# Optimization experiments

Measured on AMD Instinct MI355X. Metric: run time of the kernel, lower is better.

## Reference

```python
import jax, jax.numpy as jnp
import numpy as np

K = 5  # kernel_size per dim
# 2^dim = 4 active degree-1 B-spline products per edge (dim=2)
BITS = jnp.array([[0, 0], [1, 0], [0, 1], [1, 1]], dtype=jnp.int32)  # [S,2]


def spline_basis(edge_attr):
    """Open B-spline basis, degree=1, dim=2, kernel_size=5 per dim.
    Returns basis weights [E,S] and flattened kernel indices [E,S]."""
    v = edge_attr * (K - 1)                 # scale pseudo-coords to knot grid
    i0 = jnp.floor(v)
    f = v - i0                              # fractional part, [E,2]
    # per-dim linear weights: f for bit=1, (1-f) for bit=0
    w = jnp.where(BITS[None] == 1, f[:, None, :], 1.0 - f[:, None, :])  # [E,S,2]
    basis = w[..., 0] * w[..., 1]           # [E,S]
    idx = jnp.minimum(i0.astype(jnp.int32)[:, None, :] + BITS[None], K - 1)  # [E,S,2]
    kidx = idx[..., 0] + K * idx[..., 1]    # flatten 2D kernel index -> [0,25)
    return basis, kidx


def spline_conv(x, src, dst, basis, kidx, W, root, bias, n):
    # transform-then-gather: y[n,k,:] = x[n] @ W[k]
    y = jnp.einsum('ni,kio->nko', x, W)                 # [N,25,out]
    g = y[src[:, None], kidx]                           # gather [E,S,out]
    msg = jnp.einsum('es,eso->eo', basis, g)            # weighted sum over S
    agg = jax.ops.segment_sum(msg, dst, num_segments=n)  # scatter-add to targets
    return agg + x @ root + bias                        # root weight + bias


def setup_inputs() -> dict:
    key = jax.random.key(0)
    ks = jax.random.split(key, 8)
    N, E, IN, H, OUT = 50000, 400000, 32, 64, 64
    x = jax.random.normal(ks[0], (N, IN), jnp.float32)
    edge_index = jax.random.randint(ks[1], (2, E), 0, N, dtype=jnp.int32)
    edge_attr = jax.random.uniform(ks[2], (E, 2), jnp.float32)

    def glorot(k, shape):
        fan = shape[-2] + shape[-1]
        return jax.random.normal(k, shape, jnp.float32) * jnp.sqrt(2.0 / fan)

    W1 = glorot(ks[3], (K * K, IN, H));  root1 = glorot(ks[4], (IN, H));  b1 = jnp.zeros((H,), jnp.float32)
    W2 = glorot(ks[5], (K * K, H, OUT)); root2 = glorot(ks[6], (H, OUT)); b2 = jnp.zeros((OUT,), jnp.float32)
    fc_w = glorot(ks[7], (OUT, 3));      fc_b = jnp.zeros((3,), jnp.float32)
    return dict(x=x, edge_index=edge_index, edge_attr=edge_attr,
                W1=W1, root1=root1, b1=b1, W2=W2, root2=root2, b2=b2,
                fc_w=fc_w, fc_b=fc_b)


def reference(x, edge_index, edge_attr, W1, root1, b1, W2, root2, b2, fc_w, fc_b):
    # eval-mode forward (dropout is identity at inference)
    n = x.shape[0]
    src, dst = edge_index[0], edge_index[1]
    basis, kidx = spline_basis(edge_attr)
    h = jax.nn.relu(spline_conv(x, src, dst, basis, kidx, W1, root1, b1, n))
    h = jax.nn.relu(spline_conv(h, src, dst, basis, kidx, W2, root2, b2, n))
    return h @ fc_w + fc_b
```

## Files before the change

kernel.cpp:

```cpp
#include <hip/hip_runtime.h>
#include <stdint.h>

typedef __attribute__((ext_vector_type(8))) short short8;
typedef __attribute__((ext_vector_type(4))) float f32x4;
typedef __attribute__((ext_vector_type(4))) unsigned short ushort4v;

#define CHUNK 512

__device__ __forceinline__ unsigned short f2bf(float f) {
    unsigned int u = __float_as_uint(f);
    u = (u + 0x7FFFu + ((u >> 16) & 1u)) >> 16;
    return (unsigned short)u;
}
__device__ __forceinline__ float bf2f(unsigned short h) {
    return __uint_as_float(((unsigned int)h) << 16);
}
__device__ __forceinline__ int cell_of(float ax, float ay) {
    int c0 = (int)floorf(ax * 4.f); c0 = min(max(c0, 0), 3);
    int c1 = (int)floorf(ay * 4.f); c1 = min(max(c1, 0), 3);
    return c0 + 4 * c1;
}

__global__ __launch_bounds__(256) void zero_kernel(int* __restrict__ p, int n) {
    int t = blockIdx.x * 256 + threadIdx.x;
    if (t < n) p[t] = 0;
}

template<int KIN>
__device__ __forceinline__ void pack_cell_elem(const float* __restrict__ W,
                                               unsigned short* __restrict__ pkc, int u) {
    constexpr int KCH = KIN / 8;
    if (u >= 16 * 4 * KCH * 512) return;
    int low9 = u & 511;
    int grp  = u >> 9;
    int kc = grp % KCH; grp /= KCH;
    int c  = grp & 3;
    int cell = grp >> 2;
    int lane = low9 >> 3, j = low9 & 7;
    int k = kc * 32 + (lane >> 4) * 8 + j;
    int t = k / KIN, i = k % KIN;
    int k0 = (cell & 3) + (t & 1);   if (k0 > 4) k0 = 4;
    int k1 = (cell >> 2) + (t >> 1); if (k1 > 4) k1 = 4;
    float val = W[((size_t)(k0 + 5 * k1) * KIN + i) * 64 + (c * 16 + (lane & 15))];
    pkc[u] = f2bf(val);
}

template<int KIN>
__device__ __forceinline__ void pack_root_elem(const float* __restrict__ root,
                                               unsigned short* __restrict__ pkr, int u) {
    constexpr int KCHr = KIN / 32;
    if (u >= 4 * KCHr * 512) return;
    int low9 = u & 511;
    int grp  = u >> 9;
    int lane = low9 >> 3, j = low9 & 7;
    int kc = grp % KCHr, c = grp / KCHr;
    int k = kc * 32 + (lane >> 4) * 8 + j;
    int o = c * 16 + (lane & 15);
    float v = root[(size_t)k * 64 + o];
    unsigned short h = f2bf(v);
    pkr[(size_t)(grp * 2) * 512 + low9]     = h;
    pkr[(size_t)(grp * 2 + 1) * 512 + low9] = f2bf(v - bf2f(h));
}

__global__ __launch_bounds__(256) void prep_kernel(
    const float* __restrict__ attr, const int* __restrict__ dst,
    int* __restrict__ hist, int* __restrict__ dhist, int E,
    const float* __restrict__ W1, const float* __restrict__ W2,
    const float* __restrict__ root1, const float* __restrict__ root2,
    unsigned short* __restrict__ pkc1, unsigned short* __restrict__ pkc2,
    unsigned short* __restrict__ pkr1, unsigned short* __restrict__ pkr2,
    const float* __restrict__ x, unsigned short* __restrict__ xb, int n4,
    int EB)
{
    __shared__ int wcnt[4][16];
    int b = blockIdx.x;
    if (b < EB) {
        int e = b * 256 + threadIdx.x;
        int lane = threadIdx.x & 63, wave = threadIdx.x >> 6;
        int cell = -1;
        if (e < E) {
            float2 a = reinterpret_cast<const float2*>(attr)[e];
            cell = cell_of(a.x, a.y);
            atomicAdd(&dhist[dst[e]], 1);
        }
        #pragma unroll
        for (int c = 0; c < 16; c++) {
            unsigned long long m = __ballot(cell == c);
            if (lane == 0) wcnt[wave][c] = __popcll(m);
        }
        __syncthreads();
        if (threadIdx.x < 16) {
            int c = threadIdx.x;
            int tot = wcnt[0][c] + wcnt[1][c] + wcnt[2][c] + wcnt[3][c];
            if (tot) atomicAdd(&hist[c], tot);
        }
        return;
    }
    b -= EB;
    if (b < 512)  { pack_cell_elem<32>(W1, pkc1, b * 256 + threadIdx.x); return; }
    b -= 512;
    if (b < 1024) { pack_cell_elem<64>(W2, pkc2, b * 256 + threadIdx.x); return; }
    b -= 1024;
    if (b < 8)    { pack_root_elem<32>(root1, pkr1, b * 256 + threadIdx.x); return; }
    b -= 8;
    if (b < 16)   { pack_root_elem<64>(root2, pkr2, b * 256 + threadIdx.x); return; }
    b -= 16;
    {
        int t = b * 256 + threadIdx.x;
        if (t < n4) {
            float4 v = reinterpret_cast<const float4*>(x)[t];
            ushort4v o = { f2bf(v.x), f2bf(v.y), f2bf(v.z), f2bf(v.w) };
            reinterpret_cast<ushort4v*>(xb)[t] = o;
        }
    }
}

__global__ __launch_bounds__(1024) void scanA_kernel(const int* __restrict__ dhist,
                                                     int* __restrict__ nof,
                                                     int* __restrict__ bsum, int Np1) {
    __shared__ int wsum[16];
    int tid = threadIdx.x, lane = tid & 63, w = tid >> 6;
    int i = blockIdx.x * 1024 + tid;
    int v = (i < Np1) ? dhist[i] : 0;
    int s = v;
    #pragma unroll
    for (int off = 1; off < 64; off <<= 1) {
        int t = __shfl_up(s, off);
        if (lane >= off) s += t;
    }
    if (lane == 63) wsum[w] = s;
    __syncthreads();
    if (tid == 0) {
        int a = 0;
        #pragma unroll
        for (int k = 0; k < 16; k++) { int t = wsum[k]; wsum[k] = a; a += t; }
        bsum[blockIdx.x] = a;
    }
    __syncthreads();
    if (i < Np1) nof[i] = wsum[w] + s - v;
}

__global__ void scan_small_kernel(const int* __restrict__ hist, int* __restrict__ off_e,
                                  int* __restrict__ off_b, int* __restrict__ cursor,
                                  const int* __restrict__ bsum, int* __restrict__ bbase, int NB) {
    if (threadIdx.x == 0 && blockIdx.x == 0) {
        int se = 0, sb = 0;
        for (int c = 0; c < 16; c++) {
            off_e[c] = se; off_b[c] = sb; cursor[c] = se;
            se += hist[c]; sb += (hist[c] + CHUNK - 1) / CHUNK;
        }
        off_e[16] = se; off_b[16] = sb;
        int a = 0;
        for (int bks = 0; bks < NB; bks++) { int t = bsum[bks]; bbase[bks] = a; a += t; }
    }
}

__global__ __launch_bounds__(256) void scatter_kernel(const float* __restrict__ attr,
                                                      const int* __restrict__ src,
                                                      const int* __restrict__ dst,
                                                      const int* __restrict__ nof,
                                                      const int* __restrict__ bbase,
                                                      int4* __restrict__ emeta,
                                                      int* __restrict__ cursor,
                                                      int* __restrict__ dhist, int E) {
    __shared__ int wcnt[4][16];
    __shared__ int wbase[4][16];
    int e = blockIdx.x * 256 + threadIdx.x;
    int lane = threadIdx.x & 63, wave = threadIdx.x >> 6;
    int cell = -1;
    float2 a = {0.f, 0.f};
    int mp = 0, sv = 0;
    if (e < E) {
        a = reinterpret_cast<const float2*>(attr)[e];
        cell = cell_of(a.x, a.y);
        int d = dst[e];
        int rank = atomicSub(&dhist[d], 1) - 1;
        mp = nof[d] + bbase[d >> 10] + rank;
        sv = src[e];
    }
    int myrank = 0;
    #pragma unroll
    for (int c = 0; c < 16; c++) {
        unsigned long long m = __ballot(cell == c);
        if (cell == c) myrank = __popcll(m & ((1ull << lane) - 1ull));
        if (lane == 0) wcnt[wave][c] = __popcll(m);
    }
    __syncthreads();
    if (threadIdx.x < 16) {
        int c = threadIdx.x;
        int t0 = wcnt[0][c], t1 = wcnt[1][c], t2 = wcnt[2][c], t3 = wcnt[3][c];
        int tot = t0 + t1 + t2 + t3;
        int g = tot ? atomicAdd(&cursor[c], tot) : 0;
        wbase[0][c] = g;
        wbase[1][c] = g + t0;
        wbase[2][c] = g + t0 + t1;
        wbase[3][c] = g + t0 + t1 + t2;
    }
    __syncthreads();
    if (e < E) {
        int slot = wbase[wave][cell] + myrank;
        emeta[slot] = make_int4(sv, mp, __float_as_int(a.x), __float_as_int(a.y));
    }
}

template<int KIN>
__global__ __launch_bounds__(256) void layer_kernel(
    const unsigned short* __restrict__ Xb,
    const unsigned short* __restrict__ pkr, float* __restrict__ rt,
    const float* __restrict__ bias, int N, int RG,
    const unsigned short* __restrict__ pkc, unsigned short* __restrict__ msg,
    const int4* __restrict__ emeta,
    const int* __restrict__ off_e, const int* __restrict__ off_b)
{
    constexpr int KCHr = KIN / 32;
    constexpr int KCH  = 4 * KCHr;
    __shared__ unsigned short Blds[4 * KCH * 512];

    const int lane = threadIdx.x & 63;
    const int wave = threadIdx.x >> 6;
    const int lrow = lane & 15, lch = lane >> 4;

    if (blockIdx.x < RG) {
        const int mbase = blockIdx.x * 64 + wave * 16;
        short8 afrag[KCHr];
        {
            int row = mbase + lrow;
            if (row > N - 1) row = N - 1;
            const unsigned short* ap = Xb + (size_t)row * KIN + lch * 8;
            #pragma unroll
            for (int kc = 0; kc < KCHr; kc++)
                afrag[kc] = *reinterpret_cast<const short8*>(ap + kc * 32);
        }
        f32x4 acc[4];
        #pragma unroll
        for (int c = 0; c < 4; c++) acc[c] = (f32x4){0.f, 0.f, 0.f, 0.f};
        #pragma unroll
        for (int c = 0; c < 4; c++) {
            #pragma unroll
            for (int kc = 0; kc < KCHr; kc++) {
                short8 bh = *reinterpret_cast<const short8*>(pkr + ((size_t)(c * KCHr + kc) * 2    ) * 512 + lane * 8);
                short8 bl = *reinterpret_cast<const short8*>(pkr + ((size_t)(c * KCHr + kc) * 2 + 1) * 512 + lane * 8);
                acc[c] = __builtin_amdgcn_mfma_f32_16x16x32_bf16(afrag[kc], bh, acc[c], 0, 0, 0);
                acc[c] = __builtin_amdgcn_mfma_f32_16x16x32_bf16(afrag[kc], bl, acc[c], 0, 0, 0);
            }
        }
        #pragma unroll
        for (int c = 0; c < 4; c++) {
            int o = c * 16 + lrow;
            float bv = bias[o];
            #pragma unroll
            for (int r = 0; r < 4; r++) {
                int m = mbase + lch * 4 + r;
                if (m < N) rt[(size_t)m * 64 + o] = acc[c][r] + bv;
            }
        }
        return;
    }

    const int b = blockIdx.x - RG;
    if (b >= off_b[16]) return;
    int cell = 0;
    #pragma unroll
    for (int c = 1; c < 16; c++) cell += (b >= off_b[c]);
    const int chunk = b - off_b[cell];

    {
        const short8* sp = reinterpret_cast<const short8*>(pkc + (size_t)cell * (4 * KCH * 512));
        short8* dp = reinterpret_cast<short8*>(Blds);
        #pragma unroll
        for (int p = 0; p < (4 * KCH * 512 / 8) / 256; p++)
            dp[p * 256 + threadIdx.x] = sp[p * 256 + threadIdx.x];
    }
    __syncthreads();

    const int ebeg = off_e[cell];
    const int eend = off_e[cell + 1];
    const int base = ebeg + chunk * CHUNK;
    const float c0f = (float)(cell & 3), c1f = (float)(cell >> 2);

    for (int tt = 0; tt < 8; tt++) {
        const int tbase = base + (tt * 4 + wave) * 16;
        if (tbase >= eend) continue;
        const int eslot = tbase + lrow;
        const bool valid = eslot < eend;

        const int4 em = emeta[valid ? eslot : ebeg];
        const int s  = em.x;
        const int mp = valid ? em.y : -1;
        const float ax = __int_as_float(em.z);
        const float ay = __int_as_float(em.w);

        const float f0 = ax * 4.f - c0f;
        const float f1 = ay * 4.f - c1f;
        float w[4] = { (1.f - f0) * (1.f - f1), f0 * (1.f - f1),
                       (1.f - f0) * f1,         f0 * f1 };

        short8 xfrag[KCHr];
        {
            const unsigned short* xp = Xb + (size_t)s * KIN + lch * 8;
            #pragma unroll
            for (int kcr = 0; kcr < KCHr; kcr++)
                xfrag[kcr] = *reinterpret_cast<const short8*>(xp + kcr * 32);
        }

        float wr[4][4];
        int pv[4];
        #pragma unroll
        for (int r = 0; r < 4; r++) {
            int er = lch * 4 + r;
            #pragma unroll
            for (int t = 0; t < 4; t++) wr[t][r] = __shfl(w[t], er);
            pv[r] = __shfl(mp, er);
        }

        #pragma unroll
        for (int ch = 0; ch < 2; ch++) {
            f32x4 accT[4][2];
            #pragma unroll
            for (int t = 0; t < 4; t++)
                #pragma unroll
                for (int c2 = 0; c2 < 2; c2++)
                    accT[t][c2] = (f32x4){0.f, 0.f, 0.f, 0.f};

            #pragma unroll
            for (int t = 0; t < 4; t++) {
                #pragma unroll
                for (int kcr = 0; kcr < KCHr; kcr++) {
                    #pragma unroll
                    for (int c2 = 0; c2 < 2; c2++) {
                        int c = ch * 2 + c2;
                        short8 bf = *reinterpret_cast<const short8*>(
                            &Blds[(size_t)((c * KCH) + (t * KCHr + kcr)) * 512 + lane * 8]);
                        accT[t][c2] = __builtin_amdgcn_mfma_f32_16x16x32_bf16(xfrag[kcr], bf, accT[t][c2], 0, 0, 0);
                    }
                }
            }

            #pragma unroll
            for (int c2 = 0; c2 < 2; c2++) {
                const int o = (ch * 2 + c2) * 16 + lrow;
                #pragma unroll
                for (int r = 0; r < 4; r++) {
                    if (pv[r] >= 0) {
                        float m = wr[0][r] * accT[0][c2][r] + wr[1][r] * accT[1][c2][r]
                                + wr[2][r] * accT[2][c2][r] + wr[3][r] * accT[3][c2][r];
                        msg[(size_t)pv[r] * 64 + o] = f2bf(m);
                    }
                }
            }
        }
    }
}

template<int MODE>
__global__ __launch_bounds__(256) void segsum_kernel(
    const unsigned short* __restrict__ msg, const float* __restrict__ rt,
    const int* __restrict__ nof, const int* __restrict__ bbase,
    unsigned short* __restrict__ hout,
    const float* __restrict__ fcw, const float* __restrict__ fcb,
    float* __restrict__ out, int N)
{
    int n = blockIdx.x * 4 + (threadIdx.x >> 6);
    if (n >= N) return;
    int lane = threadIdx.x & 63;
    float acc = rt[(size_t)n * 64 + lane];
    int jb = nof[n]     + bbase[n >> 10];
    int je = nof[n + 1] + bbase[(n + 1) >> 10];
    int j = jb;
    for (; j + 3 < je; j += 4) {
        float a0 = bf2f(msg[(size_t)(j + 0) * 64 + lane]);
        float a1 = bf2f(msg[(size_t)(j + 1) * 64 + lane]);
        float a2 = bf2f(msg[(size_t)(j + 2) * 64 + lane]);
        float a3 = bf2f(msg[(size_t)(j + 3) * 64 + lane]);
        acc += a0; acc += a1; acc += a2; acc += a3;
    }
    for (; j < je; j++) acc += bf2f(msg[(size_t)j * 64 + lane]);
    acc = fmaxf(acc, 0.f);
    if (MODE == 0) {
        hout[(size_t)n * 64 + lane] = f2bf(acc);
    } else {
        float p0 = acc * fcw[lane * 3 + 0];
        float p1 = acc * fcw[lane * 3 + 1];
        float p2 = acc * fcw[lane * 3 + 2];
        #pragma unroll
        for (int off = 32; off; off >>= 1) {
            p0 += __shfl_xor(p0, off);
            p1 += __shfl_xor(p1, off);
            p2 += __shfl_xor(p2, off);
        }
        if (lane == 0) {
            out[(size_t)n * 3 + 0] = p0 + fcb[0];
            out[(size_t)n * 3 + 1] = p1 + fcb[1];
            out[(size_t)n * 3 + 2] = p2 + fcb[2];
        }
    }
}

extern "C" void kernel_launch(void* const* d_in, const int* in_sizes, int n_in,
                              void* d_out, int out_size, void* d_ws, size_t ws_size,
                              hipStream_t stream)
{
    const float* x     = (const float*)d_in[0];
    const int*   ei    = (const int*)  d_in[1];
    const float* attr  = (const float*)d_in[2];
    const float* W1    = (const float*)d_in[3];
    const float* root1 = (const float*)d_in[4];
    const float* b1    = (const float*)d_in[5];
    const float* W2    = (const float*)d_in[6];
    const float* root2 = (const float*)d_in[7];
    const float* b2    = (const float*)d_in[8];
    const float* fcw   = (const float*)d_in[9];
    const float* fcb   = (const float*)d_in[10];

    const int N = in_sizes[0] / 32;
    const int E = in_sizes[1] / 2;
    const int* srcp = ei;
    const int* dstp = ei + E;

    char* wsp = (char*)d_ws;
    auto alloc = [&](size_t bytes) -> char* {
        char* p = wsp;
        wsp += (bytes + 255) & ~(size_t)255;
        return p;
    };
    const int NB = (N + 1 + 1023) / 1024;

    float*          rt       = (float*)alloc((size_t)N * 64 * 4);
    unsigned short* xb       = (unsigned short*)alloc((size_t)N * 32 * 2);
    unsigned short* h1b      = (unsigned short*)alloc((size_t)N * 64 * 2);
    unsigned short* pkr1     = (unsigned short*)alloc((size_t)4 * 1 * 2 * 512 * 2);
    unsigned short* pkr2     = (unsigned short*)alloc((size_t)4 * 2 * 2 * 512 * 2);
    unsigned short* pkc1     = (unsigned short*)alloc((size_t)16 * 4 * 4 * 512 * 2);
    unsigned short* pkc2     = (unsigned short*)alloc((size_t)16 * 4 * 8 * 512 * 2);
    int4*           emeta    = (int4*)alloc((size_t)E * 16);
    int*            nof      = (int*)alloc((size_t)(N + 1) * 4);
    int*            bsum     = (int*)alloc((size_t)NB * 4);
    int*            bbase    = (int*)alloc((size_t)NB * 4);
    int*            off_e    = (int*)alloc(17 * 4);
    int*            off_b    = (int*)alloc(17 * 4);
    int*            cursor   = (int*)alloc(16 * 4);
    int*            zbase    = (int*)alloc((size_t)(16 + N + 1) * 4);
    int*            hist     = zbase;
    int*            dhist    = zbase + 16;
    unsigned short* msg      = (unsigned short*)alloc((size_t)E * 64 * 2);

    const int ZN = 16 + N + 1;
    zero_kernel<<<(ZN + 255) / 256, 256, 0, stream>>>(zbase, ZN);

    const int EB = (E + 255) / 256;
    const int CB = (N * 8 + 255) / 256;
    const int prep_grid = EB + 512 + 1024 + 8 + 16 + CB;

    prep_kernel<<<prep_grid, 256, 0, stream>>>(attr, dstp, hist, dhist, E,
                                               W1, W2, root1, root2,
                                               pkc1, pkc2, pkr1, pkr2,
                                               x, xb, N * 8, EB);
    scanA_kernel<<<NB, 1024, 0, stream>>>(dhist, nof, bsum, N + 1);
    scan_small_kernel<<<1, 64, 0, stream>>>(hist, off_e, off_b, cursor, bsum, bbase, NB);
    scatter_kernel<<<EB, 256, 0, stream>>>(attr, srcp, dstp, nof, bbase, emeta, cursor, dhist, E);

    const int RG = (N + 63) / 64;
    const int lgrid = RG + (E + CHUNK - 1) / CHUNK + 16;
    const int sgrid = (N + 3) / 4;

    layer_kernel<32><<<lgrid, 256, 0, stream>>>(xb, pkr1, rt, b1, N, RG,
                                                pkc1, msg, emeta, off_e, off_b);
    segsum_kernel<0><<<sgrid, 256, 0, stream>>>(msg, rt, nof, bbase, h1b, fcw, fcb, (float*)d_out, N);

    layer_kernel<64><<<lgrid, 256, 0, stream>>>(h1b, pkr2, rt, b2, N, RG,
                                                pkc2, msg, emeta, off_e, off_b);
    segsum_kernel<1><<<sgrid, 256, 0, stream>>>(msg, rt, nof, bbase, nullptr, fcw, fcb, (float*)d_out, N);
}
```

Before: 181.4 us.

## Process two edge tiles per wave iteration, double chunk size, fuse scan kernels

The layer kernel now handles two 16-edge tiles per wave iteration, so each B fragment loaded from LDS feeds two MFMAs. The chunk size grows to 1024 edges per block to amortise the per-block weight staging into LDS. The two scan kernels are merged into one, using a last-block-done atomic counter, which removes a kernel launch. The trade-off is higher register pressure from the doubled accumulators and fragments, and fewer, larger blocks that may leave some cells underfilled.

```diff
diff --git a/kernel.cpp b/kernel.cpp
--- a/kernel.cpp
+++ b/kernel.cpp
@@ -5,7 +5,7 @@
 typedef __attribute__((ext_vector_type(4))) float f32x4;
 typedef __attribute__((ext_vector_type(4))) unsigned short ushort4v;
 
-#define CHUNK 512
+#define CHUNK 1024
 
 __device__ __forceinline__ unsigned short f2bf(float f) {
     unsigned int u = __float_as_uint(f);
@@ -115,9 +115,12 @@
     }
 }
 
-__global__ __launch_bounds__(1024) void scanA_kernel(const int* __restrict__ dhist,
-                                                     int* __restrict__ nof,
-                                                     int* __restrict__ bsum, int Np1) {
+__global__ __launch_bounds__(1024) void scanAB_kernel(
+    const int* __restrict__ dhist, int* __restrict__ nof, int* __restrict__ bsum,
+    int Np1, int* __restrict__ done,
+    const int* __restrict__ hist, int* __restrict__ off_e, int* __restrict__ off_b,
+    int* __restrict__ cursor, int* __restrict__ bbase, int NB)
+{
     __shared__ int wsum[16];
     int tid = threadIdx.x, lane = tid & 63, w = tid >> 6;
     int i = blockIdx.x * 1024 + tid;
@@ -138,20 +141,27 @@
     }
     __syncthreads();
     if (i < Np1) nof[i] = wsum[w] + s - v;
-}
-
-__global__ void scan_small_kernel(const int* __restrict__ hist, int* __restrict__ off_e,
-                                  int* __restrict__ off_b, int* __restrict__ cursor,
-                                  const int* __restrict__ bsum, int* __restrict__ bbase, int NB) {
-    if (threadIdx.x == 0 && blockIdx.x == 0) {
+
+    __shared__ int amLast;
+    __shared__ int lds_b[256];
+    __shared__ int lds_h[16];
+    __threadfence();
+    if (tid == 0) amLast = (atomicAdd(done, 1) == gridDim.x - 1);
+    __syncthreads();
+    if (!amLast) return;
+    __threadfence();
+    if (tid < NB) lds_b[tid] = bsum[tid];
+    if (tid < 16) lds_h[tid] = hist[tid];
+    __syncthreads();
+    if (tid == 0) {
+        int a = 0;
+        for (int k = 0; k < NB; k++) { int t = lds_b[k]; bbase[k] = a; a += t; }
         int se = 0, sb = 0;
         for (int c = 0; c < 16; c++) {
             off_e[c] = se; off_b[c] = sb; cursor[c] = se;
-            se += hist[c]; sb += (hist[c] + CHUNK - 1) / CHUNK;
+            se += lds_h[c]; sb += (lds_h[c] + CHUNK - 1) / CHUNK;
         }
         off_e[16] = se; off_b[16] = sb;
-        int a = 0;
-        for (int bks = 0; bks < NB; bks++) { int t = bsum[bks]; bbase[bks] = a; a += t; }
     }
 }
 
@@ -278,74 +288,87 @@
     const int base = ebeg + chunk * CHUNK;
     const float c0f = (float)(cell & 3), c1f = (float)(cell >> 2);
 
-    for (int tt = 0; tt < 8; tt++) {
-        const int tbase = base + (tt * 4 + wave) * 16;
-        if (tbase >= eend) continue;
-        const int eslot = tbase + lrow;
-        const bool valid = eslot < eend;
-
-        const int4 em = emeta[valid ? eslot : ebeg];
-        const int s  = em.x;
-        const int mp = valid ? em.y : -1;
-        const float ax = __int_as_float(em.z);
-        const float ay = __int_as_float(em.w);
-
-        const float f0 = ax * 4.f - c0f;
-        const float f1 = ay * 4.f - c1f;
-        float w[4] = { (1.f - f0) * (1.f - f1), f0 * (1.f - f1),
-                       (1.f - f0) * f1,         f0 * f1 };
-
-        short8 xfrag[KCHr];
+    for (int it = 0; it < CHUNK / 128; it++) {
+        const int tbase = base + (it * 4 + wave) * 32;
+        if (tbase >= eend) break;
+        const int slA = tbase + lrow;
+        const int slB = tbase + 16 + lrow;
+        const bool vA = slA < eend;
+        const bool vB = slB < eend;
+
+        const int4 emA = emeta[vA ? slA : ebeg];
+        const int4 emB = emeta[vB ? slB : ebeg];
+        const int sA = emA.x, sB = emB.x;
+        const int mpA = vA ? emA.y : -1;
+        const int mpB = vB ? emB.y : -1;
+
+        float wAv[4], wBv[4];
         {
-            const unsigned short* xp = Xb + (size_t)s * KIN + lch * 8;
-            #pragma unroll
-            for (int kcr = 0; kcr < KCHr; kcr++)
-                xfrag[kcr] = *reinterpret_cast<const short8*>(xp + kcr * 32);
-        }
-
-        float wr[4][4];
-        int pv[4];
+            float f0 = __int_as_float(emA.z) * 4.f - c0f;
+            float f1 = __int_as_float(emA.w) * 4.f - c1f;
+            wAv[0] = (1.f - f0) * (1.f - f1); wAv[1] = f0 * (1.f - f1);
+            wAv[2] = (1.f - f0) * f1;         wAv[3] = f0 * f1;
+            f0 = __int_as_float(emB.z) * 4.f - c0f;
+            f1 = __int_as_float(emB.w) * 4.f - c1f;
+            wBv[0] = (1.f - f0) * (1.f - f1); wBv[1] = f0 * (1.f - f1);
+            wBv[2] = (1.f - f0) * f1;         wBv[3] = f0 * f1;
+        }
+
+        short8 xfA[KCHr], xfB[KCHr];
+        {
+            const unsigned short* xpA = Xb + (size_t)sA * KIN + lch * 8;
+            const unsigned short* xpB = Xb + (size_t)sB * KIN + lch * 8;
+            #pragma unroll
+            for (int kcr = 0; kcr < KCHr; kcr++) {
+                xfA[kcr] = *reinterpret_cast<const short8*>(xpA + kcr * 32);
+                xfB[kcr] = *reinterpret_cast<const short8*>(xpB + kcr * 32);
+            }
+        }
+
+        float wrA[4][4], wrB[4][4];
+        int pvA[4], pvB[4];
         #pragma unroll
         for (int r = 0; r < 4; r++) {
             int er = lch * 4 + r;
             #pragma unroll
-            for (int t = 0; t < 4; t++) wr[t][r] = __shfl(w[t], er);
-            pv[r] = __shfl(mp, er);
-        }
-
-        #pragma unroll
-        for (int ch = 0; ch < 2; ch++) {
-            f32x4 accT[4][2];
-            #pragma unroll
-            for (int t = 0; t < 4; t++)
-                #pragma unroll
-                for (int c2 = 0; c2 < 2; c2++)
-                    accT[t][c2] = (f32x4){0.f, 0.f, 0.f, 0.f};
-
+            for (int t = 0; t < 4; t++) {
+                wrA[t][r] = __shfl(wAv[t], er);
+                wrB[t][r] = __shfl(wBv[t], er);
+            }
+            pvA[r] = __shfl(mpA, er);
+            pvB[r] = __shfl(mpB, er);
+        }
+
+        #pragma unroll
+        for (int c = 0; c < 4; c++) {
+            f32x4 accA[4], accB[4];
+            #pragma unroll
+            for (int t = 0; t < 4; t++) {
+                accA[t] = (f32x4){0.f, 0.f, 0.f, 0.f};
+                accB[t] = (f32x4){0.f, 0.f, 0.f, 0.f};
+            }
             #pragma unroll
             for (int t = 0; t < 4; t++) {
                 #pragma unroll
                 for (int kcr = 0; kcr < KCHr; kcr++) {
-                    #pragma unroll
-                    for (int c2 = 0; c2 < 2; c2++) {
-                        int c = ch * 2 + c2;
-                        short8 bf = *reinterpret_cast<const short8*>(
-                            &Blds[(size_t)((c * KCH) + (t * KCHr + kcr)) * 512 + lane * 8]);
-                        accT[t][c2] = __builtin_amdgcn_mfma_f32_16x16x32_bf16(xfrag[kcr], bf, accT[t][c2], 0, 0, 0);
-                    }
+                    short8 bf = *reinterpret_cast<const short8*>(
+                        &Blds[(size_t)((c * KCH) + (t * KCHr + kcr)) * 512 + lane * 8]);
+                    accA[t] = __builtin_amdgcn_mfma_f32_16x16x32_bf16(xfA[kcr], bf, accA[t], 0, 0, 0);
+                    accB[t] = __builtin_amdgcn_mfma_f32_16x16x32_bf16(xfB[kcr], bf, accB[t], 0, 0, 0);
                 }
             }
-
-            #pragma unroll
-            for (int c2 = 0; c2 < 2; c2++) {
-                const int o = (ch * 2 + c2) * 16 + lrow;
-                #pragma unroll
-                for (int r = 0; r < 4; r++) {
-                    if (pv[r] >= 0) {
-                        float m = wr[0][r] * accT[0][c2][r] + wr[1][r] * accT[1][c2][r]
-                                + wr[2][r] * accT[2][c2][r] + wr[3][r] * accT[3][c2][r];
-                        msg[(size_t)pv[r] * 64 + o] = f2bf(m);
-                    }
+            const int o = c * 16 + lrow;
+            #pragma unroll
+            for (int r = 0; r < 4; r++) {
+                if (pvA[r] >= 0) {
+                    float m = wrA[0][r] * accA[0][r] + wrA[1][r] * accA[1][r]
+                            + wrA[2][r] * accA[2][r] + wrA[3][r] * accA[3][r];
+                    msg[(size_t)pvA[r] * 64 + o] = f2bf(m);
+                }
+                if (pvB[r] >= 0) {
+                    float m = wrB[0][r] * accB[0][r] + wrB[1][r] * accB[1][r]
+                            + wrB[2][r] * accB[2][r] + wrB[3][r] * accB[3][r];
+                    msg[(size_t)pvB[r] * 64 + o] = f2bf(m);
                 }
             }
         }
@@ -439,12 +462,13 @@
     int*            off_e    = (int*)alloc(17 * 4);
     int*            off_b    = (int*)alloc(17 * 4);
     int*            cursor   = (int*)alloc(16 * 4);
-    int*            zbase    = (int*)alloc((size_t)(16 + N + 1) * 4);
+    int*            zbase    = (int*)alloc((size_t)(16 + N + 1 + 1) * 4);
     int*            hist     = zbase;
     int*            dhist    = zbase + 16;
+    int*            done     = zbase + 16 + N + 1;
     unsigned short* msg      = (unsigned short*)alloc((size_t)E * 64 * 2);
 
-    const int ZN = 16 + N + 1;
+    const int ZN = 16 + N + 1 + 1;
     zero_kernel<<<(ZN + 255) / 256, 256, 0, stream>>>(zbase, ZN);
 
     const int EB = (E + 255) / 256;
@@ -455,8 +479,8 @@
                                                W1, W2, root1, root2,
                                                pkc1, pkc2, pkr1, pkr2,
                                                x, xb, N * 8, EB);
-    scanA_kernel<<<NB, 1024, 0, stream>>>(dhist, nof, bsum, N + 1);
-    scan_small_kernel<<<1, 64, 0, stream>>>(hist, off_e, off_b, cursor, bsum, bbase, NB);
+    scanAB_kernel<<<NB, 1024, 0, stream>>>(dhist, nof, bsum, N + 1, done,
+                                           hist, off_e, off_b, cursor, bbase, NB);
     scatter_kernel<<<EB, 256, 0, stream>>>(attr, srcp, dstp, nof, bbase, emeta, cursor, dhist, E);
 
     const int RG = (N + 63) / 64;
```

Measured after the change: 213.0 us. 17.4% more time.
